# Kernel optimization log

Measured on AMD Instinct MI355X. Metric: run time of the kernel, lower is better.

Reference implementation:

```python
import jax, jax.numpy as jnp
import numpy as np

B, S, D = 2, 2048, 1024
H, HD = 16, 64          # num_heads, head_dim = D // H
W = 31                  # window_size (odd)
E = 1024                # embed_dim


def setup_inputs() -> dict:
    key = jax.random.key(0)
    ks = jax.random.split(key, 12)
    sd = 1.0 / np.sqrt(D)
    so = 1.0 / np.sqrt(H * HD)
    return {
        "x": jax.random.normal(ks[0], (B, S, D), jnp.float32),
        "fsq": jax.random.normal(ks[1], (1, S, D), jnp.float32),   # feature_squeeze_token
        "pos": jax.random.normal(ks[2], (1, S, D), jnp.float32),   # position_token
        "Wq": jax.random.normal(ks[3], (H, D, HD), jnp.float32) * sd,
        "bq": jax.random.normal(ks[4], (H, HD), jnp.float32) * sd,
        "Wk": jax.random.normal(ks[5], (H, D, HD), jnp.float32) * sd,
        "bk": jax.random.normal(ks[6], (H, HD), jnp.float32) * sd,
        "Wv": jax.random.normal(ks[7], (H, D, HD), jnp.float32) * sd,
        "bv": jax.random.normal(ks[8], (H, HD), jnp.float32) * sd,
        "Wo": jax.random.normal(ks[9], (H * HD, E), jnp.float32) * so,
        "bo": jax.random.normal(ks[10], (E,), jnp.float32) * so,
    }


def reference(x, fsq, pos, Wq, bq, Wk, bk, Wv, bv, Wo, bo):
    b, s, d = x.shape
    pad = (W - 1) // 2
    # sliding windows: (B, S, W, D), zero-padded at sequence edges
    xp = jnp.pad(x, ((0, 0), (pad, pad), (0, 0)))
    idx = jnp.arange(s)[:, None] + jnp.arange(W)[None, :]  # (S, W)
    win = xp[:, idx, :]  # (B, S, W, D)
    a = jnp.broadcast_to(fsq[:, :, None, :], (b, s, 1, d))  # squeeze token per pos
    bt = jnp.broadcast_to(pos[:, :, None, :], (b, s, 1, d))  # position token per pos
    kv = jnp.concatenate([win, bt, a], axis=2)  # (B, S, K=W+2, D)
    q = jnp.broadcast_to(fsq, (b, s, d))        # query = squeeze token
    # per-head projections (heads stacked on axis h)
    qh = jnp.einsum("bsd,hde->bhse", q, Wq) + bq[None, :, None, :]        # (B,H,S,HD)
    kh = jnp.einsum("bskd,hde->bhske", kv, Wk) + bk[None, :, None, None, :]
    vh = jnp.einsum("bskd,hde->bhske", kv, Wv) + bv[None, :, None, None, :]
    scores = jnp.einsum("bhse,bhske->bhsk", qh, kh) / jnp.sqrt(jnp.asarray(HD, x.dtype))
    attn = jax.nn.softmax(scores, axis=-1)  # dropout is identity in eval
    outh = jnp.einsum("bhsk,bhske->bhse", attn, vh)  # (B,H,S,HD)
    concat = outh.transpose(0, 2, 1, 3).reshape(b, s, H * HD)  # heads concat order 0..H-1
    return concat @ Wo + bo  # (B, S, E)
```

## Files before the change

kernel.cpp:

```cpp
#include <hip/hip_runtime.h>


typedef __attribute__((ext_vector_type(8))) short bf16x8;
typedef __attribute__((ext_vector_type(4))) float f32x4;
typedef unsigned short u16;
typedef unsigned int u32;

__device__ __forceinline__ float bf2f(u16 u) {
  union { u32 i; float f; } v; v.i = ((u32)u) << 16; return v.f;
}
__device__ __forceinline__ u16 f2bf(float f) {
  union { float f; u32 i; } v; v.f = f;
  u32 r = v.i + 0x7fffu + ((v.i >> 16) & 1u);
  return (u16)(r >> 16);
}
__device__ __forceinline__ float2 unpk(u32 u) {
  union { u32 i; float f; } lo, hi;
  lo.i = u << 16; hi.i = u & 0xffff0000u;
  return make_float2(lo.f, hi.f);
}
__device__ __forceinline__ float dot8(uint4 a, uint4 b) {
  float s = 0.f;
  { float2 x = unpk(a.x), y = unpk(b.x); s += x.x*y.x + x.y*y.y; }
  { float2 x = unpk(a.y), y = unpk(b.y); s += x.x*y.x + x.y*y.y; }
  { float2 x = unpk(a.z), y = unpk(b.z); s += x.x*y.x + x.y*y.y; }
  { float2 x = unpk(a.w), y = unpk(b.w); s += x.x*y.x + x.y*y.y; }
  return s;
}
__device__ __forceinline__ void gload_lds16(const u16* g, u16* l) {
  __builtin_amdgcn_global_load_lds((const __attribute__((address_space(1))) void*)(g),
                                   (__attribute__((address_space(3))) void*)(l),
                                   16, 0, 0);
}
__device__ __forceinline__ uint4 pack8(float4 a, float4 b) {
  union { u16 h[8]; uint4 q; } u;
  u.h[0] = f2bf(a.x); u.h[1] = f2bf(a.y); u.h[2] = f2bf(a.z); u.h[3] = f2bf(a.w);
  u.h[4] = f2bf(b.x); u.h[5] = f2bf(b.y); u.h[6] = f2bf(b.z); u.h[7] = f2bf(b.w);
  return u.q;
}

__global__ __launch_bounds__(256) void f2b8(const float* __restrict__ in,
                                            u16* __restrict__ out, int n8) {
  int i = blockIdx.x * 256 + threadIdx.x;
  if (i >= n8) return;
  float4 a = ((const float4*)in)[2 * i];
  float4 b = ((const float4*)in)[2 * i + 1];
  ((uint4*)out)[i] = pack8(a, b);
}

__device__ __forceinline__ void transpose_body(const float* src, u16* dst,
                                               int R, int C) {
  __shared__ u16 tile[64][72];
  int r0 = blockIdx.y * 64, c0 = blockIdx.x * 64;
  int t = threadIdx.x;
#pragma unroll
  for (int i = 0; i < 16; ++i) {
    int idx = i * 256 + t;
    int r = idx >> 6, c = idx & 63;
    tile[r][c] = f2bf(src[(size_t)(r0 + r) * C + (c0 + c)]);
  }
  __syncthreads();
#pragma unroll
  for (int i = 0; i < 16; ++i) {
    int idx = i * 256 + t;
    int c = idx >> 6, r = idx & 63;
    dst[(size_t)(c0 + c) * R + (r0 + r)] = tile[r][c];
  }
}

__global__ __launch_bounds__(256) void transpose64_f2b(const float* __restrict__ in,
                                                       u16* __restrict__ out,
                                                       int R, int C) {
  const size_t zoff = (size_t)blockIdx.z * R * C;
  transpose_body(in + zoff, out + zoff, R, C);
}

__global__ __launch_bounds__(256) void transposeQKV(const float* __restrict__ Wq,
                                                    const float* __restrict__ Wk,
                                                    const float* __restrict__ Wv,
                                                    u16* __restrict__ WqT,
                                                    u16* __restrict__ WkT,
                                                    u16* __restrict__ WvT) {
  int z = blockIdx.z;
  const float* src; u16* dst;
  if (z < 16)      { src = Wq; dst = WqT; }
  else if (z < 32) { src = Wk; dst = WkT; }
  else             { src = Wv; dst = WvT; }
  const size_t zoff = (size_t)(z & 15) * 1024 * 64;
  transpose_body(src + zoff, dst + zoff, 1024, 64);
}

template <bool OUTF32>
__device__ __forceinline__ void gemm_body(const u16* __restrict__ Ap,
                                          const u16* __restrict__ BT,
                                          const float* __restrict__ bias,
                                          void* Cp, int tile_n) {
  __shared__ u16 As[128 * 32];
  __shared__ u16 Bs[128 * 32];
  const int t = threadIdx.x, lane = t & 63, wave = t >> 6;
  const int wm = (wave >> 1) * 64, wn = (wave & 1) * 64;
  const int row16 = lane & 15, quad = lane >> 4;
  const int srow = wave * 32 + (lane >> 2);
  const int scol = (lane & 3) * 8;

  f32x4 acc[4][4] = {};

  for (int k0 = 0; k0 < 1024; k0 += 32) {
    __syncthreads();
    gload_lds16(Ap + (size_t)srow * 1024 + k0 + scol, &As[wave * 1024]);
    gload_lds16(Ap + (size_t)(srow + 16) * 1024 + k0 + scol, &As[wave * 1024 + 512]);
    gload_lds16(BT + (size_t)(tile_n + srow) * 1024 + k0 + scol, &Bs[wave * 1024]);
    gload_lds16(BT + (size_t)(tile_n + srow + 16) * 1024 + k0 + scol, &Bs[wave * 1024 + 512]);
    __syncthreads();

    bf16x8 a_frag[4], b_frag[4];
#pragma unroll
    for (int i = 0; i < 4; ++i)
      a_frag[i] = *(const bf16x8*)(&As[(wm + i * 16 + row16) * 32 + quad * 8]);
#pragma unroll
    for (int j = 0; j < 4; ++j)
      b_frag[j] = *(const bf16x8*)(&Bs[(wn + j * 16 + row16) * 32 + quad * 8]);
#pragma unroll
    for (int i = 0; i < 4; ++i)
#pragma unroll
      for (int j = 0; j < 4; ++j)
        acc[i][j] = __builtin_amdgcn_mfma_f32_16x16x32_bf16(
            a_frag[i], b_frag[j], acc[i][j], 0, 0, 0);
  }

#pragma unroll
  for (int j = 0; j < 4; ++j) {
    int n = tile_n + wn + j * 16 + row16;
    float bb = bias[n];
#pragma unroll
    for (int i = 0; i < 4; ++i) {
      int m0 = wm + i * 16 + quad * 4;
#pragma unroll
      for (int r = 0; r < 4; ++r) {
        float val = acc[i][j][r] + bb;
        if (OUTF32) ((float*)Cp)[(size_t)(m0 + r) * 1024 + n] = val;
        else        ((u16*)Cp)[(size_t)(m0 + r) * 1024 + n] = f2bf(val);
      }
    }
  }
}

__global__ __launch_bounds__(256) void proj_gemm(const u16* __restrict__ xb,
                                                 const u16* __restrict__ fsqb,
                                                 const u16* __restrict__ posb,
                                                 const u16* __restrict__ WkT,
                                                 const u16* __restrict__ WvT,
                                                 const u16* __restrict__ WqT,
                                                 const float* __restrict__ bk,
                                                 const float* __restrict__ bv,
                                                 const float* __restrict__ bq,
                                                 u16* __restrict__ Kp,
                                                 u16* __restrict__ Vp,
                                                 u16* __restrict__ Qp) {
  int bid = blockIdx.x;
  const u16* Ap; const u16* BT; const float* bias; u16* C; int tile_n;
  if (bid < 1024) {
    int tm = bid >> 4, tn = bid & 15;
    if (tm < 32)      Ap = xb   + (size_t)tm * 128 * 1024;
    else if (tm < 48) Ap = fsqb + (size_t)(tm - 32) * 128 * 1024;
    else              Ap = posb + (size_t)(tm - 48) * 128 * 1024;
    if (tn < 8) { BT = WkT; bias = bk; C = Kp + (size_t)tm * 128 * 1024; tile_n = tn * 128; }
    else        { BT = WvT; bias = bv; C = Vp + (size_t)tm * 128 * 1024; tile_n = (tn - 8) * 128; }
  } else {
    int q = bid - 1024; int tm = q >> 3; tile_n = (q & 7) * 128;
    Ap = fsqb + (size_t)tm * 128 * 1024; BT = WqT; bias = bq;
    C = Qp + (size_t)tm * 128 * 1024;
  }
  gemm_body<false>(Ap, BT, bias, C, tile_n);
}

__global__ __launch_bounds__(256) void out_gemm(const u16* __restrict__ Att,
                                                const u16* __restrict__ WoT,
                                                const float* __restrict__ bo,
                                                float* __restrict__ Out) {
  int tile_n = blockIdx.x * 128, tm = blockIdx.y;
  gemm_body<true>(Att + (size_t)tm * 128 * 1024, WoT, bo,
                  Out + (size_t)tm * 128 * 1024, tile_n);
}

#define AST 72
#define QS  0
#define KWS 2304
#define VTS 6912
#define KPS 11520
#define PS  20736

__global__ __launch_bounds__(256) void attn_tile(const u16* __restrict__ Qp,
                                                 const u16* __restrict__ Kp,
                                                 const u16* __restrict__ Vp,
                                                 const float* __restrict__ bk,
                                                 const float* __restrict__ bv,
                                                 u16* __restrict__ Att) {
  __shared__ u16 sm[23040];
  __shared__ float smP[32 * 68];

  const int t = threadIdx.x;
  const int bid = blockIdx.x;
  const int s0 = (bid & 63) * 32;
  const int h  = (bid >> 6) & 15;
  const int b  = bid >> 10;
  const int lane = t & 63, wave = t >> 6;
  const int row16 = lane & 15, quad = lane >> 4;
  const int hcol = h * 64;

  { int w = t >> 3, oct = t & 7;
    *(uint4*)&sm[QS + w * AST + oct * 8] =
        *(const uint4*)(Qp + (size_t)(s0 + w) * 1024 + hcol + oct * 8); }
#pragma unroll
  for (int i = 0; i < 2; ++i) {
    int task = i * 256 + t; int w = task >> 3, oct = task & 7;
    int g = s0 + w - 15;
    uint4 v;
    if ((unsigned)g < 2048u)
      v = *(const uint4*)(Kp + (size_t)(b * 2048 + g) * 1024 + hcol + oct * 8);
    else
      v = pack8(*(const float4*)(bk + hcol + oct * 8),
                *(const float4*)(bk + hcol + oct * 8 + 4));
    *(uint4*)&sm[KWS + w * AST + oct * 8] = v;
  }
#pragma unroll
  for (int i = 0; i < 4; ++i) {
    int task = i * 256 + t;
    int which = task >> 8, r = (task >> 3) & 31, oct = task & 7;
    const u16* src = (which < 2) ? Kp : Vp;
    size_t grow = ((which & 1) == 0) ? (size_t)(6144 + s0 + r)
                                     : (size_t)(4096 + s0 + r);
    *(uint4*)&sm[KPS + which * 2304 + r * AST + oct * 8] =
        *(const uint4*)(src + grow * 1024 + hcol + oct * 8);
  }
#pragma unroll
  for (int i = 0; i < 2; ++i) {
    int task = i * 256 + t; int w = task >> 3, oct = task & 7;
    int g = s0 + w - 15;
    union { u16 h8[8]; uint4 q; } u;
    if ((unsigned)g < 2048u)
      u.q = *(const uint4*)(Vp + (size_t)(b * 2048 + g) * 1024 + hcol + oct * 8);
    else
      u.q = pack8(*(const float4*)(bv + hcol + oct * 8),
                  *(const float4*)(bv + hcol + oct * 8 + 4));
#pragma unroll
    for (int j = 0; j < 8; ++j)
      sm[VTS + (oct * 8 + j) * AST + w] = u.h8[j];
  }
  __syncthreads();

  {
    f32x4 accS[2] = {};
#pragma unroll
    for (int kc = 0; kc < 2; ++kc) {
      bf16x8 bf_ = *(const bf16x8*)&sm[KWS + (wave * 16 + row16) * AST + kc * 32 + quad * 8];
#pragma unroll
      for (int mi = 0; mi < 2; ++mi) {
        bf16x8 af = *(const bf16x8*)&sm[QS + (mi * 16 + row16) * AST + kc * 32 + quad * 8];
        accS[mi] = __builtin_amdgcn_mfma_f32_16x16x32_bf16(af, bf_, accS[mi], 0, 0, 0);
      }
    }
#pragma unroll
    for (int mi = 0; mi < 2; ++mi)
#pragma unroll
      for (int r = 0; r < 4; ++r) {
        int s = mi * 16 + quad * 4 + r;
        int w = wave * 16 + row16;
        float v = accS[mi][r] * 0.125f;
        smP[s * 68 + w] = (w >= s && w <= s + 30) ? v : -1e30f;
      }
  }
  if (t < 64) {
    int s = t >> 1, which = t & 1;
    int base = KPS + which * 2304;
    float a = 0.f;
#pragma unroll
    for (int c = 0; c < 8; ++c)
      a += dot8(*(const uint4*)&sm[QS + s * AST + c * 8],
                *(const uint4*)&sm[base + s * AST + c * 8]);
    smP[s * 68 + 64 + which] = a * 0.125f;
  }
  __syncthreads();

  if (t < 32) {
    int s = t;
    float vals[33];
#pragma unroll
    for (int k = 0; k < 31; ++k) vals[k] = smP[s * 68 + s + k];
    vals[31] = smP[s * 68 + 64];
    vals[32] = smP[s * 68 + 65];
    float mx = -1e30f;
#pragma unroll
    for (int k = 0; k < 33; ++k) mx = fmaxf(mx, vals[k]);
    float sum = 0.f;
#pragma unroll
    for (int k = 0; k < 33; ++k) { vals[k] = __expf(vals[k] - mx); sum += vals[k]; }
    float inv = 1.f / sum;
    u32* prow = (u32*)&sm[PS + s * AST];
#pragma unroll
    for (int j = 0; j < 32; ++j) prow[j] = 0;
#pragma unroll
    for (int k = 0; k < 31; ++k)
      sm[PS + s * AST + s + k] = f2bf(vals[k] * inv);
    smP[s * 68 + 66] = vals[31] * inv;
    smP[s * 68 + 67] = vals[32] * inv;
  }
  __syncthreads();

  {
    f32x4 accO[2] = {};
#pragma unroll
    for (int kc = 0; kc < 2; ++kc) {
      bf16x8 bf_ = *(const bf16x8*)&sm[VTS + (wave * 16 + row16) * AST + kc * 32 + quad * 8];
#pragma unroll
      for (int mi = 0; mi < 2; ++mi) {
        bf16x8 af = *(const bf16x8*)&sm[PS + (mi * 16 + row16) * AST + kc * 32 + quad * 8];
        accO[mi] = __builtin_amdgcn_mfma_f32_16x16x32_bf16(af, bf_, accO[mi], 0, 0, 0);
      }
    }
#pragma unroll
    for (int mi = 0; mi < 2; ++mi)
#pragma unroll
      for (int r = 0; r < 4; ++r) {
        int s = mi * 16 + quad * 4 + r;
        int e = wave * 16 + row16;
        float o = accO[mi][r]
                + smP[s * 68 + 66] * bf2f(sm[KPS + 2 * 2304 + s * AST + e])
                + smP[s * 68 + 67] * bf2f(sm[KPS + 3 * 2304 + s * AST + e]);
        Att[(size_t)(b * 2048 + s0 + s) * 1024 + hcol + e] = f2bf(o);
      }
  }
}

extern "C" void kernel_launch(void* const* d_in, const int* in_sizes, int n_in,
                              void* d_out, int out_size, void* d_ws, size_t ws_size,
                              hipStream_t stream) {
  (void)in_sizes; (void)n_in; (void)out_size; (void)ws_size;

  const float* x   = (const float*)d_in[0];
  const float* fsq = (const float*)d_in[1];
  const float* pos = (const float*)d_in[2];
  const float* Wq  = (const float*)d_in[3];
  const float* bq  = (const float*)d_in[4];
  const float* Wk  = (const float*)d_in[5];
  const float* bk  = (const float*)d_in[6];
  const float* Wv  = (const float*)d_in[7];
  const float* bv  = (const float*)d_in[8];
  const float* Wo  = (const float*)d_in[9];
  const float* bo  = (const float*)d_in[10];

  u16* ws = (u16*)d_ws;
  const size_t M1 = 1024 * 1024;
  u16* WqT  = ws + 0 * M1;
  u16* WkT  = ws + 1 * M1;
  u16* WvT  = ws + 2 * M1;
  u16* WoT  = ws + 3 * M1;
  u16* Qp   = ws + 4 * M1;
  u16* Kp   = ws + 6 * M1;
  u16* Vp   = ws + 14 * M1;
  u16* fsqb = ws + 22 * M1;
  u16* posb = ws + 24 * M1;
  u16* xb   = ws + 26 * M1;
  u16* Att  = ws + 22 * M1;

  f2b8<<<2048, 256, 0, stream>>>(x, xb, 524288);
  f2b8<<<1024, 256, 0, stream>>>(fsq, fsqb, 262144);
  f2b8<<<1024, 256, 0, stream>>>(pos, posb, 262144);

  transposeQKV<<<dim3(1, 16, 48), 256, 0, stream>>>(Wq, Wk, Wv, WqT, WkT, WvT);
  transpose64_f2b<<<dim3(16, 16, 1), 256, 0, stream>>>(Wo, WoT, 1024, 1024);

  proj_gemm<<<1152, 256, 0, stream>>>(xb, fsqb, posb, WkT, WvT, WqT,
                                      bk, bv, bq, Kp, Vp, Qp);

  attn_tile<<<2048, 256, 0, stream>>>(Qp, Kp, Vp, bk, bv, Att);

  out_gemm<<<dim3(8, 32), 256, 0, stream>>>(Att, WoT, bo, (float*)d_out);
}
```

Measured before the change: 230.8 us.

## Merge conversion/transpose launches, deepen GEMM K-tile with swizzled LDS, compact scores

The three fp32-to-bf16 conversion kernels become one launch, and the four weight transposes become one launch. The shared GEMM body now stages 64-wide K tiles instead of 32, halving the barrier count, and uses an XOR-swizzled LDS layout to avoid bank conflicts on fragment reads. The attention kernel stores only the 31 in-window scores per row in a compact buffer instead of a masked 64-wide row. The trade-off is larger LDS use per GEMM block, which may lower occupancy, plus extra swizzle address arithmetic.

Result: faster. 214.0 us (-7.3%).

```diff
diff --git a/kernel.cpp b/kernel.cpp
--- a/kernel.cpp
+++ b/kernel.cpp
@@ -39,19 +39,25 @@
   return u.q;
 }
 
-__global__ __launch_bounds__(256) void f2b8(const float* __restrict__ in,
-                                            u16* __restrict__ out, int n8) {
+__global__ __launch_bounds__(256) void f2b_all(const float* __restrict__ x,
+                                               const float* __restrict__ fsq,
+                                               const float* __restrict__ pos,
+                                               u16* __restrict__ xb,
+                                               u16* __restrict__ fsqb,
+                                               u16* __restrict__ posb) {
   int i = blockIdx.x * 256 + threadIdx.x;
-  if (i >= n8) return;
-  float4 a = ((const float4*)in)[2 * i];
-  float4 b = ((const float4*)in)[2 * i + 1];
-  ((uint4*)out)[i] = pack8(a, b);
+  const float* src; u16* dst; int off;
+  if (i < 524288)      { src = x;   dst = xb;   off = i; }
+  else if (i < 786432) { src = fsq; dst = fsqb; off = i - 524288; }
+  else                 { src = pos; dst = posb; off = i - 786432; }
+  float4 a = ((const float4*)src)[2 * off];
+  float4 b = ((const float4*)src)[2 * off + 1];
+  ((uint4*)dst)[off] = pack8(a, b);
 }
 
 __device__ __forceinline__ void transpose_body(const float* src, u16* dst,
-                                               int R, int C) {
+                                               int R, int C, int r0, int c0) {
   __shared__ u16 tile[64][72];
-  int r0 = blockIdx.y * 64, c0 = blockIdx.x * 64;
   int t = threadIdx.x;
 #pragma unroll
   for (int i = 0; i < 16; ++i) {
@@ -68,26 +74,27 @@
   }
 }
 
-__global__ __launch_bounds__(256) void transpose64_f2b(const float* __restrict__ in,
-                                                       u16* __restrict__ out,
-                                                       int R, int C) {
-  const size_t zoff = (size_t)blockIdx.z * R * C;
-  transpose_body(in + zoff, out + zoff, R, C);
-}
-
-__global__ __launch_bounds__(256) void transposeQKV(const float* __restrict__ Wq,
-                                                    const float* __restrict__ Wk,
-                                                    const float* __restrict__ Wv,
-                                                    u16* __restrict__ WqT,
-                                                    u16* __restrict__ WkT,
-                                                    u16* __restrict__ WvT) {
+__global__ __launch_bounds__(256) void transpose_all(const float* __restrict__ Wq,
+                                                     const float* __restrict__ Wk,
+                                                     const float* __restrict__ Wv,
+                                                     const float* __restrict__ Wo,
+                                                     u16* __restrict__ WqT,
+                                                     u16* __restrict__ WkT,
+                                                     u16* __restrict__ WvT,
+                                                     u16* __restrict__ WoT) {
   int z = blockIdx.z;
-  const float* src; u16* dst;
-  if (z < 16)      { src = Wq; dst = WqT; }
-  else if (z < 32) { src = Wk; dst = WkT; }
-  else             { src = Wv; dst = WvT; }
-  const size_t zoff = (size_t)(z & 15) * 1024 * 64;
-  transpose_body(src + zoff, dst + zoff, 1024, 64);
+  if (z < 3) {
+    const float* s = (z == 0) ? Wq : (z == 1) ? Wk : Wv;
+    u16* d = (z == 0) ? WqT : (z == 1) ? WkT : WvT;
+    size_t off = (size_t)blockIdx.x * 65536;
+    transpose_body(s + off, d + off, 1024, 64, blockIdx.y * 64, 0);
+  } else {
+    transpose_body(Wo, WoT, 1024, 1024, blockIdx.y * 64, blockIdx.x * 64);
+  }
+}
+
+__device__ __forceinline__ int swz(int R, int c) {
+  return (R * 8 + (c ^ (R & 7))) * 8;
 }
 
 template <bool OUTF32>
@@ -95,37 +102,44 @@
                                           const u16* __restrict__ BT,
                                           const float* __restrict__ bias,
                                           void* Cp, int tile_n) {
-  __shared__ u16 As[128 * 32];
-  __shared__ u16 Bs[128 * 32];
+  __shared__ u16 As[128 * 64];
+  __shared__ u16 Bs[128 * 64];
   const int t = threadIdx.x, lane = t & 63, wave = t >> 6;
   const int wm = (wave >> 1) * 64, wn = (wave & 1) * 64;
   const int row16 = lane & 15, quad = lane >> 4;
-  const int srow = wave * 32 + (lane >> 2);
-  const int scol = (lane & 3) * 8;
+  const int l8 = lane >> 3;
+  const int cswz = (lane & 7) ^ l8;
 
   f32x4 acc[4][4] = {};
 
-  for (int k0 = 0; k0 < 1024; k0 += 32) {
+  for (int k0 = 0; k0 < 1024; k0 += 64) {
     __syncthreads();
-    gload_lds16(Ap + (size_t)srow * 1024 + k0 + scol, &As[wave * 1024]);
-    gload_lds16(Ap + (size_t)(srow + 16) * 1024 + k0 + scol, &As[wave * 1024 + 512]);
-    gload_lds16(BT + (size_t)(tile_n + srow) * 1024 + k0 + scol, &Bs[wave * 1024]);
-    gload_lds16(BT + (size_t)(tile_n + srow + 16) * 1024 + k0 + scol, &Bs[wave * 1024 + 512]);
+#pragma unroll
+    for (int j = 0; j < 4; ++j) {
+      int r = wave * 32 + j * 8 + l8;
+      gload_lds16(Ap + (size_t)r * 1024 + k0 + cswz * 8,
+                  &As[wave * 2048 + j * 512]);
+      gload_lds16(BT + (size_t)(tile_n + r) * 1024 + k0 + cswz * 8,
+                  &Bs[wave * 2048 + j * 512]);
+    }
     __syncthreads();
 
-    bf16x8 a_frag[4], b_frag[4];
-#pragma unroll
-    for (int i = 0; i < 4; ++i)
-      a_frag[i] = *(const bf16x8*)(&As[(wm + i * 16 + row16) * 32 + quad * 8]);
-#pragma unroll
-    for (int j = 0; j < 4; ++j)
-      b_frag[j] = *(const bf16x8*)(&Bs[(wn + j * 16 + row16) * 32 + quad * 8]);
-#pragma unroll
-    for (int i = 0; i < 4; ++i)
+#pragma unroll
+    for (int kb = 0; kb < 2; ++kb) {
+      bf16x8 a_frag[4], b_frag[4];
+#pragma unroll
+      for (int i = 0; i < 4; ++i)
+        a_frag[i] = *(const bf16x8*)&As[swz(wm + i * 16 + row16, kb * 4 + quad)];
 #pragma unroll
       for (int j = 0; j < 4; ++j)
-        acc[i][j] = __builtin_amdgcn_mfma_f32_16x16x32_bf16(
-            a_frag[i], b_frag[j], acc[i][j], 0, 0, 0);
+        b_frag[j] = *(const bf16x8*)&Bs[swz(wn + j * 16 + row16, kb * 4 + quad)];
+#pragma unroll
+      for (int i = 0; i < 4; ++i)
+#pragma unroll
+        for (int j = 0; j < 4; ++j)
+          acc[i][j] = __builtin_amdgcn_mfma_f32_16x16x32_bf16(
+              a_frag[i], b_frag[j], acc[i][j], 0, 0, 0);
+    }
   }
 
 #pragma unroll
@@ -197,7 +211,7 @@
                                                  const float* __restrict__ bv,
                                                  u16* __restrict__ Att) {
   __shared__ u16 sm[23040];
-  __shared__ float smP[32 * 68];
+  __shared__ float smP[32 * 36];
 
   const int t = threadIdx.x;
   const int bid = blockIdx.x;
@@ -266,8 +280,8 @@
       for (int r = 0; r < 4; ++r) {
         int s = mi * 16 + quad * 4 + r;
         int w = wave * 16 + row16;
-        float v = accS[mi][r] * 0.125f;
-        smP[s * 68 + w] = (w >= s && w <= s + 30) ? v : -1e30f;
+        int d = w - s;
+        if (d >= 0 && d <= 30) smP[s * 36 + d] = accS[mi][r] * 0.125f;
       }
   }
   if (t < 64) {
@@ -278,7 +292,7 @@
     for (int c = 0; c < 8; ++c)
       a += dot8(*(const uint4*)&sm[QS + s * AST + c * 8],
                 *(const uint4*)&sm[base + s * AST + c * 8]);
-    smP[s * 68 + 64 + which] = a * 0.125f;
+    smP[s * 36 + 31 + which] = a * 0.125f;
   }
   __syncthreads();
 
@@ -286,9 +300,7 @@
     int s = t;
     float vals[33];
 #pragma unroll
-    for (int k = 0; k < 31; ++k) vals[k] = smP[s * 68 + s + k];
-    vals[31] = smP[s * 68 + 64];
-    vals[32] = smP[s * 68 + 65];
+    for (int k = 0; k < 33; ++k) vals[k] = smP[s * 36 + k];
     float mx = -1e30f;
 #pragma unroll
     for (int k = 0; k < 33; ++k) mx = fmaxf(mx, vals[k]);
@@ -302,8 +314,8 @@
 #pragma unroll
     for (int k = 0; k < 31; ++k)
       sm[PS + s * AST + s + k] = f2bf(vals[k] * inv);
-    smP[s * 68 + 66] = vals[31] * inv;
-    smP[s * 68 + 67] = vals[32] * inv;
+    smP[s * 36 + 33] = vals[31] * inv;
+    smP[s * 36 + 34] = vals[32] * inv;
   }
   __syncthreads();
 
@@ -325,8 +337,8 @@
         int s = mi * 16 + quad * 4 + r;
         int e = wave * 16 + row16;
         float o = accO[mi][r]
-                + smP[s * 68 + 66] * bf2f(sm[KPS + 2 * 2304 + s * AST + e])
-                + smP[s * 68 + 67] * bf2f(sm[KPS + 3 * 2304 + s * AST + e]);
+                + smP[s * 36 + 33] * bf2f(sm[KPS + 2 * 2304 + s * AST + e])
+                + smP[s * 36 + 34] * bf2f(sm[KPS + 3 * 2304 + s * AST + e]);
         Att[(size_t)(b * 2048 + s0 + s) * 1024 + hcol + e] = f2bf(o);
       }
   }
@@ -363,12 +375,9 @@
   u16* xb   = ws + 26 * M1;
   u16* Att  = ws + 22 * M1;
 
-  f2b8<<<2048, 256, 0, stream>>>(x, xb, 524288);
-  f2b8<<<1024, 256, 0, stream>>>(fsq, fsqb, 262144);
-  f2b8<<<1024, 256, 0, stream>>>(pos, posb, 262144);
-
-  transposeQKV<<<dim3(1, 16, 48), 256, 0, stream>>>(Wq, Wk, Wv, WqT, WkT, WvT);
-  transpose64_f2b<<<dim3(16, 16, 1), 256, 0, stream>>>(Wo, WoT, 1024, 1024);
+  f2b_all<<<4096, 256, 0, stream>>>(x, fsq, pos, xb, fsqb, posb);
+  transpose_all<<<dim3(16, 16, 4), 256, 0, stream>>>(Wq, Wk, Wv, Wo,
+                                                     WqT, WkT, WvT, WoT);
 
   proj_gemm<<<1152, 256, 0, stream>>>(xb, fsqb, posb, WkT, WvT, WqT,
                                       bk, bv, bq, Kp, Vp, Qp);
```
